# Kernel tuning notes

Hardware: AMD Instinct MI355X
Metric: run time of the kernel (lower is better)

## Reference

```python
import jax, jax.numpy as jnp
import numpy as np

N = 50000   # nodes
E = 800000  # edges (before self loops)
D = 128     # feature dim (n_feat == all n_units due to fusion-cat constraint)
BN_EPS = 1e-5


def _gcn_norm(edge_index, edge_weight, n):
    # PyG gcn_norm with add_self_loops=True (self-loop weight 1.0)
    loop = jnp.arange(n)
    row = jnp.concatenate([edge_index[0], loop])
    col = jnp.concatenate([edge_index[1], loop])
    w = jnp.concatenate([edge_weight, jnp.ones((n,), edge_weight.dtype)])
    deg = jax.ops.segment_sum(w, col, num_segments=n)  # [N]
    deg_safe = jnp.where(deg > 0, deg, 1.0)
    dis = jnp.where(deg > 0, jax.lax.rsqrt(deg_safe), 0.0)
    norm = dis[row] * w * dis[col]  # [E+N]
    return row, col, norm


def _gcn_conv(x, row, col, norm, W, b):
    # out_i = sum_{j->i} norm_ij * (x_j @ W) + b
    h = x @ W                                   # [N, Dout]
    msg = norm[:, None] * h[row]                # gather + scale, [E+N, Dout]
    out = jax.ops.segment_sum(msg, col, num_segments=x.shape[0])
    return out + b


def setup_inputs() -> dict:
    key = jax.random.key(0)
    ks = jax.random.split(key, 9)
    emb = jax.random.normal(ks[0], (N, D), jnp.float32)
    edge_index = jax.random.randint(ks[1], (2, E), 0, N)
    edge_weight = jax.random.uniform(ks[2], (E,), jnp.float32)
    W0 = jax.random.normal(ks[3], (D, D), jnp.float32) / np.sqrt(D).astype(np.float32)
    b0 = jnp.zeros((D,), jnp.float32)
    W1 = jax.random.normal(ks[4], (D, D), jnp.float32) / np.sqrt(D).astype(np.float32)
    b1 = jnp.zeros((D,), jnp.float32)
    bn_gamma = jax.random.uniform(ks[5], (D,), jnp.float32, 0.5, 1.5)
    bn_beta = jax.random.normal(ks[6], (D,), jnp.float32) * 0.1
    bn_mean = jax.random.normal(ks[7], (D,), jnp.float32) * 0.1
    bn_var = jax.random.uniform(ks[8], (D,), jnp.float32, 0.5, 1.5)
    return dict(emb=emb, edge_index=edge_index, edge_weight=edge_weight,
                W0=W0, b0=b0, W1=W1, b1=b1,
                bn_gamma=bn_gamma, bn_beta=bn_beta, bn_mean=bn_mean, bn_var=bn_var)


def reference(emb, edge_index, edge_weight, W0, b0, W1, b1,
              bn_gamma, bn_beta, bn_mean, bn_var):
    n = emb.shape[0]
    row, col, norm = _gcn_norm(edge_index, edge_weight, n)
    # loop runs once (batchnorm_stack has len 1 -> zip truncates):
    h1 = _gcn_conv(emb, row, col, norm, W0, b0)
    h1 = (h1 - bn_mean) * jax.lax.rsqrt(bn_var + BN_EPS) * bn_gamma + bn_beta
    h1 = jax.nn.elu(h1)  # dropout is identity in eval mode
    # final layer applied outside loop, no BN/ELU:
    h2 = _gcn_conv(h1, row, col, norm, W1, b1)
    # fusion: mean over [emb, h1, h2] along the stacked scale axis
    return (emb + h1 + h2) / 3.0
```

## Files before the change

kernel.cpp:

```cpp
#include <hip/hip_runtime.h>
#include <hip/hip_fp16.h>
#include <math.h>

#define BN_EPS 1e-5f
#define CAP 48
#define W_SCALE 68719476736.0f

typedef __attribute__((ext_vector_type(8))) short bf16x8;
typedef __attribute__((ext_vector_type(4))) float f32x4;

__device__ __forceinline__ unsigned short f2b(float f) {
    unsigned u = __float_as_uint(f);
    return (unsigned short)((u + 0x7fffu + ((u >> 16) & 1u)) >> 16);
}
__device__ __forceinline__ unsigned pack2(float lo, float hi) {
    return (unsigned)f2b(lo) | ((unsigned)f2b(hi) << 16);
}
__device__ __forceinline__ float slot_w(unsigned s) {
    return __half2float(__ushort_as_half((unsigned short)(s & 0xffffu)));
}
__device__ __forceinline__ float4 b2f4(ushort4 u) {
    return make_float4(__uint_as_float((unsigned)u.x << 16),
                       __uint_as_float((unsigned)u.y << 16),
                       __uint_as_float((unsigned)u.z << 16),
                       __uint_as_float((unsigned)u.w << 16));
}

__global__ __launch_bounds__(256) void k_prep(
        const int* __restrict__ erow, const int* __restrict__ ecol,
        const float* __restrict__ ew,
        unsigned long long* __restrict__ packed,
        unsigned* __restrict__ eEdge, int E, int SB,
        const float* __restrict__ W0, const float* __restrict__ W1,
        const float* __restrict__ emb,
        unsigned short* __restrict__ wp0, unsigned short* __restrict__ wp1,
        unsigned short* __restrict__ embB, int n) {
    int bb = blockIdx.x;
    if (bb < SB) {
        int e0 = (bb * 256 + threadIdx.x) * 4;
        if (e0 >= E) return;
        if (e0 + 3 < E) {
            int4 r4 = *(const int4*)(erow + e0);
            int4 c4 = *(const int4*)(ecol + e0);
            float4 w4 = *(const float4*)(ew + e0);
            unsigned long long i0 = (1ull << 44) | (unsigned long long)(w4.x * W_SCALE);
            unsigned long long i1 = (1ull << 44) | (unsigned long long)(w4.y * W_SCALE);
            unsigned long long i2 = (1ull << 44) | (unsigned long long)(w4.z * W_SCALE);
            unsigned long long i3 = (1ull << 44) | (unsigned long long)(w4.w * W_SCALE);
            unsigned h0 = __half_as_ushort(__float2half(w4.x));
            unsigned h1 = __half_as_ushort(__float2half(w4.y));
            unsigned h2 = __half_as_ushort(__float2half(w4.z));
            unsigned h3 = __half_as_ushort(__float2half(w4.w));
            unsigned p0 = (unsigned)(atomicAdd(&packed[(size_t)c4.x * 8], i0) >> 44);
            unsigned p1 = (unsigned)(atomicAdd(&packed[(size_t)c4.y * 8], i1) >> 44);
            unsigned p2 = (unsigned)(atomicAdd(&packed[(size_t)c4.z * 8], i2) >> 44);
            unsigned p3 = (unsigned)(atomicAdd(&packed[(size_t)c4.w * 8], i3) >> 44);
            if (p0 < CAP) eEdge[(size_t)c4.x * CAP + p0] = ((unsigned)r4.x << 16) | h0;
            if (p1 < CAP) eEdge[(size_t)c4.y * CAP + p1] = ((unsigned)r4.y << 16) | h1;
            if (p2 < CAP) eEdge[(size_t)c4.z * CAP + p2] = ((unsigned)r4.z << 16) | h2;
            if (p3 < CAP) eEdge[(size_t)c4.w * CAP + p3] = ((unsigned)r4.w << 16) | h3;
        } else {
            for (int e = e0; e < E; ++e) {
                int r = erow[e], c = ecol[e];
                float wv = ew[e];
                unsigned long long inc = (1ull << 44) | (unsigned long long)(wv * W_SCALE);
                unsigned hb = __half_as_ushort(__float2half(wv));
                unsigned p = (unsigned)(atomicAdd(&packed[(size_t)c * 8], inc) >> 44);
                if (p < CAP) eEdge[(size_t)c * CAP + p] = ((unsigned)r << 16) | hb;
            }
        }
    } else {
        int b = bb - SB;
        if (b < 16) {
            int tid = b * 256 + threadIdx.x;
            const float* W = (tid < 2048) ? W0 : W1;
            unsigned short* wp = (tid < 2048) ? wp0 : wp1;
            int f = tid & 2047;
            int q = f >> 9;
            int t = (f >> 6) & 7;
            int l = f & 63;
            int col = t * 16 + (l & 15);
            int k0 = q * 32 + (l >> 4) * 8;
            unsigned short o[8];
            #pragma unroll
            for (int j = 0; j < 8; ++j) o[j] = f2b(W[(k0 + j) * 128 + col]);
            *(uint4*)(wp + (size_t)f * 8) = *(uint4*)o;
        } else {
            int idx = (b - 16) * 256 + threadIdx.x;
            if (idx < n * 16) {
                const float4* src = (const float4*)emb + (size_t)idx * 2;
                float4 v0 = src[0], v1 = src[1];
                uint4 o;
                o.x = pack2(v0.x, v0.y); o.y = pack2(v0.z, v0.w);
                o.z = pack2(v1.x, v1.y); o.w = pack2(v1.z, v1.w);
                ((uint4*)embB)[idx] = o;
            }
        }
    }
}

__global__ __launch_bounds__(256) void k_dis(const unsigned long long* __restrict__ packed,
                                             float* __restrict__ dis,
                                             int* __restrict__ cnt, int n) {
    int i = blockIdx.x * 256 + threadIdx.x;
    if (i >= n) return;
    unsigned long long pk = packed[(size_t)i * 8];
    int c = (int)(pk >> 44);
    if (c > CAP) c = CAP;
    float deg = (float)((double)(pk & ((1ull << 44) - 1)) * (1.0 / 68719476736.0));
    dis[i] = rsqrtf(deg + 1.0f);
    cnt[i] = c;
}

__device__ __forceinline__ void agg_node(const unsigned* __restrict__ ep,
                                         const unsigned short* __restrict__ h,
                                         const float* __restrict__ dis,
                                         float disc, int c, int lane,
                                         float acc[8]) {
    int g = lane >> 4;
    int fo = (lane & 15) * 8;
    for (int j = 0; j < c; j += 16) {
        unsigned s[4];
        int r[4];
        float d[4], nm[4];
        uint4 u[4];
        #pragma unroll
        for (int k = 0; k < 4; ++k) s[k] = ep[j + 4 * k + g];
        #pragma unroll
        for (int k = 0; k < 4; ++k) r[k] = (j + 4 * k + g < c) ? (int)(s[k] >> 16) : 0;
        #pragma unroll
        for (int k = 0; k < 4; ++k) d[k] = dis[r[k]];
        #pragma unroll
        for (int k = 0; k < 4; ++k) u[k] = *(const uint4*)(h + ((size_t)r[k] << 7) + fo);
        #pragma unroll
        for (int k = 0; k < 4; ++k)
            nm[k] = (j + 4 * k + g < c) ? d[k] * slot_w(s[k]) * disc : 0.f;
        #pragma unroll
        for (int k = 0; k < 4; ++k) {
            acc[0] += nm[k] * __uint_as_float(u[k].x << 16);
            acc[1] += nm[k] * __uint_as_float(u[k].x & 0xffff0000u);
            acc[2] += nm[k] * __uint_as_float(u[k].y << 16);
            acc[3] += nm[k] * __uint_as_float(u[k].y & 0xffff0000u);
            acc[4] += nm[k] * __uint_as_float(u[k].z << 16);
            acc[5] += nm[k] * __uint_as_float(u[k].z & 0xffff0000u);
            acc[6] += nm[k] * __uint_as_float(u[k].w << 16);
            acc[7] += nm[k] * __uint_as_float(u[k].w & 0xffff0000u);
        }
    }
    #pragma unroll
    for (int f = 0; f < 8; ++f) {
        acc[f] += __shfl_xor(acc[f], 16);
        acc[f] += __shfl_xor(acc[f], 32);
    }
}

__global__ __launch_bounds__(1024) void k_conv1(
        const int* __restrict__ cnt, const unsigned* __restrict__ eEdge,
        const unsigned short* __restrict__ embB, const float* __restrict__ dis,
        const unsigned short* __restrict__ wp,
        const float* __restrict__ b0, const float* __restrict__ gamma,
        const float* __restrict__ beta, const float* __restrict__ mean,
        const float* __restrict__ var,
        unsigned short* __restrict__ h1b, int n) {
    __shared__ unsigned short sWp[16384];
    __shared__ unsigned short sA[16 * 136];
    int t = threadIdx.x;
    { uint4* d = (uint4*)sWp; const uint4* s = (const uint4*)wp;
      d[t] = s[t]; d[t + 1024] = s[t + 1024]; }
    int w = t >> 6;
    int lane = t & 63;
    int wid = blockIdx.x * 16 + w;
    bool valid = wid < n;
    int c = valid ? __builtin_amdgcn_readfirstlane(cnt[wid]) : 0;
    float disc = valid ? dis[wid] : 0.f;
    float acc[8] = {};
    agg_node(eEdge + (size_t)wid * CAP, embB, dis, disc, c, lane, acc);
    if (lane < 16) {
        int fo = lane * 8;
        float s2 = disc * disc;
        uint4 hu = make_uint4(0, 0, 0, 0);
        if (valid) hu = *(const uint4*)(embB + ((size_t)wid << 7) + fo);
        acc[0] += s2 * __uint_as_float(hu.x << 16);
        acc[1] += s2 * __uint_as_float(hu.x & 0xffff0000u);
        acc[2] += s2 * __uint_as_float(hu.y << 16);
        acc[3] += s2 * __uint_as_float(hu.y & 0xffff0000u);
        acc[4] += s2 * __uint_as_float(hu.z << 16);
        acc[5] += s2 * __uint_as_float(hu.z & 0xffff0000u);
        acc[6] += s2 * __uint_as_float(hu.w << 16);
        acc[7] += s2 * __uint_as_float(hu.w & 0xffff0000u);
        uint4 o;
        o.x = pack2(acc[0], acc[1]); o.y = pack2(acc[2], acc[3]);
        o.z = pack2(acc[4], acc[5]); o.w = pack2(acc[6], acc[7]);
        *(uint4*)(sA + w * 136 + fo) = o;
    }
    __syncthreads();
    int m = lane & 15, quad = lane >> 4;
    f32x4 c2 = {0.f, 0.f, 0.f, 0.f};
    if (w < 8) {
        #pragma unroll
        for (int q = 0; q < 4; ++q) {
            bf16x8 a = *(const bf16x8*)(sA + m * 136 + q * 32 + quad * 8);
            bf16x8 b = *(const bf16x8*)(sWp + (size_t)((q * 8 + w) * 64 + lane) * 8);
            c2 = __builtin_amdgcn_mfma_f32_16x16x32_bf16(a, b, c2, 0, 0, 0);
        }
    }
    __syncthreads();
    if (w < 8) {
        int col = w * 16 + m;
        float bias = b0[col];
        float mn = mean[col], bt = beta[col];
        float iv = rsqrtf(var[col] + BN_EPS) * gamma[col];
        #pragma unroll
        for (int r = 0; r < 4; ++r) {
            float x = c2[r] + bias;
            x = (x - mn) * iv + bt;
            x = x > 0.f ? x : expm1f(x);
            sA[(quad * 4 + r) * 136 + col] = f2b(x);
        }
    }
    __syncthreads();
    if (t < 256) {
        int r = t >> 4, c8 = (t & 15) * 8;
        int node = blockIdx.x * 16 + r;
        if (node < n)
            *(uint4*)(h1b + ((size_t)node << 7) + c8) = *(const uint4*)(sA + r * 136 + c8);
    }
}

__global__ __launch_bounds__(1024) void k_conv2(
        const int* __restrict__ cnt, const unsigned* __restrict__ eEdge,
        const unsigned short* __restrict__ h1b, const float* __restrict__ dis,
        const unsigned short* __restrict__ wp,
        const float* __restrict__ b1, const float* __restrict__ emb,
        float* __restrict__ out, int n) {
    __shared__ unsigned short sWp[16384];
    __shared__ unsigned short sA[16 * 136];
    __shared__ float sC[16 * 132];
    int t = threadIdx.x;
    { uint4* d = (uint4*)sWp; const uint4* s = (const uint4*)wp;
      d[t] = s[t]; d[t + 1024] = s[t + 1024]; }
    int w = t >> 6;
    int lane = t & 63;
    int wid = blockIdx.x * 16 + w;
    bool valid = wid < n;
    int c = valid ? __builtin_amdgcn_readfirstlane(cnt[wid]) : 0;
    float disc = valid ? dis[wid] : 0.f;
    float acc[8] = {};
    agg_node(eEdge + (size_t)wid * CAP, h1b, dis, disc, c, lane, acc);
    if (lane < 16) {
        int fo = lane * 8;
        float s2 = disc * disc;
        uint4 hu = make_uint4(0, 0, 0, 0);
        if (valid) hu = *(const uint4*)(h1b + ((size_t)wid << 7) + fo);
        acc[0] += s2 * __uint_as_float(hu.x << 16);
        acc[1] += s2 * __uint_as_float(hu.x & 0xffff0000u);
        acc[2] += s2 * __uint_as_float(hu.y << 16);
        acc[3] += s2 * __uint_as_float(hu.y & 0xffff0000u);
        acc[4] += s2 * __uint_as_float(hu.z << 16);
        acc[5] += s2 * __uint_as_float(hu.z & 0xffff0000u);
        acc[6] += s2 * __uint_as_float(hu.w << 16);
        acc[7] += s2 * __uint_as_float(hu.w & 0xffff0000u);
        uint4 o;
        o.x = pack2(acc[0], acc[1]); o.y = pack2(acc[2], acc[3]);
        o.z = pack2(acc[4], acc[5]); o.w = pack2(acc[6], acc[7]);
        *(uint4*)(sA + w * 136 + fo) = o;
    }
    __syncthreads();
    int m = lane & 15, quad = lane >> 4;
    f32x4 c2 = {0.f, 0.f, 0.f, 0.f};
    if (w < 8) {
        #pragma unroll
        for (int q = 0; q < 4; ++q) {
            bf16x8 a = *(const bf16x8*)(sA + m * 136 + q * 32 + quad * 8);
            bf16x8 b = *(const bf16x8*)(sWp + (size_t)((q * 8 + w) * 64 + lane) * 8);
            c2 = __builtin_amdgcn_mfma_f32_16x16x32_bf16(a, b, c2, 0, 0, 0);
        }
        int col = w * 16 + m;
        float bias = b1[col];
        #pragma unroll
        for (int r = 0; r < 4; ++r)
            sC[(quad * 4 + r) * 132 + col] = c2[r] + bias;
    }
    __syncthreads();
    if (t < 512) {
        int r = t >> 5, c4 = (t & 31) * 4;
        int node = blockIdx.x * 16 + r;
        if (node < n) {
            float4 cc = *(const float4*)(sC + r * 132 + c4);
            float4 ev = *(const float4*)(emb + ((size_t)node << 7) + c4);
            float4 hv = b2f4(*(const ushort4*)(h1b + ((size_t)node << 7) + c4));
            const float third = 1.0f / 3.0f;
            float4 o;
            o.x = (ev.x + hv.x + cc.x) * third;
            o.y = (ev.y + hv.y + cc.y) * third;
            o.z = (ev.z + hv.z + cc.z) * third;
            o.w = (ev.w + hv.w + cc.w) * third;
            *(float4*)(out + ((size_t)node << 7) + c4) = o;
        }
    }
}

extern "C" void kernel_launch(void* const* d_in, const int* in_sizes, int n_in,
                              void* d_out, int out_size, void* d_ws, size_t ws_size,
                              hipStream_t stream) {
    const float* emb   = (const float*)d_in[0];
    const int*   eidx  = (const int*)d_in[1];
    const float* ew    = (const float*)d_in[2];
    const float* W0    = (const float*)d_in[3];
    const float* b0    = (const float*)d_in[4];
    const float* W1    = (const float*)d_in[5];
    const float* b1    = (const float*)d_in[6];
    const float* gamma = (const float*)d_in[7];
    const float* beta  = (const float*)d_in[8];
    const float* mean  = (const float*)d_in[9];
    const float* var   = (const float*)d_in[10];

    const int n = in_sizes[0] / 128;
    const int E = in_sizes[2];
    const int* rowp = eidx;
    const int* colp = eidx + E;

    char* ws = (char*)d_ws;
    unsigned short* embB = (unsigned short*)ws;
    unsigned short* h1b  = (unsigned short*)(ws + (size_t)n * 256);
    char* p = ws + (size_t)n * 512;
    unsigned long long* packed = (unsigned long long*)p;
    float* dis  = (float*)(p + (size_t)n * 64);
    int*   cnt  = (int*)  (p + (size_t)n * 68);
    unsigned short* wp0 = (unsigned short*)(p + (size_t)n * 72);
    unsigned short* wp1 = (unsigned short*)(p + (size_t)n * 72 + 32768);
    unsigned* eEdge = (unsigned*)(p + (size_t)n * 72 + 65536);
    float* outf = (float*)d_out;

    hipMemsetAsync(packed, 0, (size_t)n * 64, stream);

    const int nb = (n + 255) / 256;
    const int SB = (E + 1023) / 1024;
    const int PB = 16 + (n * 16 + 255) / 256;
    const int cb = (n + 15) / 16;

    k_prep<<<SB + PB, 256, 0, stream>>>(rowp, colp, ew, packed, eEdge, E, SB,
                                        W0, W1, emb, wp0, wp1, embB, n);
    k_dis<<<nb, 256, 0, stream>>>(packed, dis, cnt, n);
    k_conv1<<<cb, 1024, 0, stream>>>(cnt, eEdge, embB, dis, wp0,
                                     b0, gamma, beta, mean, var, h1b, n);
    k_conv2<<<cb, 1024, 0, stream>>>(cnt, eEdge, h1b, dis, wp1,
                                     b1, emb, outf, n);
}
```

Before: 242.4 us.

## Replace global-atomic edge bucketing with two-pass LDS binning by destination block

Edge preprocessing no longer scatters into per-node slots with 64-bit global atomics. It first bins each chunk of edges by destination node block (256 nodes) using a shared-memory histogram and prefix scan. A second kernel then builds per-node edge lists and weighted degrees with LDS atomics, one block per node bin. This drops the memset and the separate degree kernel and aims to cut contended global atomics, at the cost of an extra pass over the binned edge records, which reuse the h1 buffer. The degree is now summed in float rather than fixed-point, so its summation order is nondeterministic.

```diff
diff --git a/kernel.cpp b/kernel.cpp
--- a/kernel.cpp
+++ b/kernel.cpp
@@ -4,7 +4,7 @@
 
 #define BN_EPS 1e-5f
 #define CAP 48
-#define W_SCALE 68719476736.0f
+#define ABLK 8192
 
 typedef __attribute__((ext_vector_type(8))) short bf16x8;
 typedef __attribute__((ext_vector_type(4))) float f32x4;
@@ -26,67 +26,100 @@
                        __uint_as_float((unsigned)u.w << 16));
 }
 
-__global__ __launch_bounds__(256) void k_prep(
+__global__ __launch_bounds__(1024) void k_bin(
         const int* __restrict__ erow, const int* __restrict__ ecol,
         const float* __restrict__ ew,
-        unsigned long long* __restrict__ packed,
-        unsigned* __restrict__ eEdge, int E, int SB,
+        uint2* __restrict__ binned, unsigned short* __restrict__ Hs,
+        int E, int NA, int nbins,
         const float* __restrict__ W0, const float* __restrict__ W1,
         const float* __restrict__ emb,
         unsigned short* __restrict__ wp0, unsigned short* __restrict__ wp1,
         unsigned short* __restrict__ embB, int n) {
     int bb = blockIdx.x;
-    if (bb < SB) {
-        int e0 = (bb * 256 + threadIdx.x) * 4;
-        if (e0 >= E) return;
-        if (e0 + 3 < E) {
-            int4 r4 = *(const int4*)(erow + e0);
-            int4 c4 = *(const int4*)(ecol + e0);
-            float4 w4 = *(const float4*)(ew + e0);
-            unsigned long long i0 = (1ull << 44) | (unsigned long long)(w4.x * W_SCALE);
-            unsigned long long i1 = (1ull << 44) | (unsigned long long)(w4.y * W_SCALE);
-            unsigned long long i2 = (1ull << 44) | (unsigned long long)(w4.z * W_SCALE);
-            unsigned long long i3 = (1ull << 44) | (unsigned long long)(w4.w * W_SCALE);
-            unsigned h0 = __half_as_ushort(__float2half(w4.x));
-            unsigned h1 = __half_as_ushort(__float2half(w4.y));
-            unsigned h2 = __half_as_ushort(__float2half(w4.z));
-            unsigned h3 = __half_as_ushort(__float2half(w4.w));
-            unsigned p0 = (unsigned)(atomicAdd(&packed[(size_t)c4.x * 8], i0) >> 44);
-            unsigned p1 = (unsigned)(atomicAdd(&packed[(size_t)c4.y * 8], i1) >> 44);
-            unsigned p2 = (unsigned)(atomicAdd(&packed[(size_t)c4.z * 8], i2) >> 44);
-            unsigned p3 = (unsigned)(atomicAdd(&packed[(size_t)c4.w * 8], i3) >> 44);
-            if (p0 < CAP) eEdge[(size_t)c4.x * CAP + p0] = ((unsigned)r4.x << 16) | h0;
-            if (p1 < CAP) eEdge[(size_t)c4.y * CAP + p1] = ((unsigned)r4.y << 16) | h1;
-            if (p2 < CAP) eEdge[(size_t)c4.z * CAP + p2] = ((unsigned)r4.z << 16) | h2;
-            if (p3 < CAP) eEdge[(size_t)c4.w * CAP + p3] = ((unsigned)r4.w << 16) | h3;
+    int t = threadIdx.x;
+    if (bb < NA) {
+        __shared__ unsigned sHist[256];
+        __shared__ unsigned sStart[257];
+        __shared__ unsigned sCur[256];
+        if (t < 256) sHist[t] = 0;
+        __syncthreads();
+        int base = bb * ABLK;
+        int m = E - base; if (m > ABLK) m = ABLK;
+        int er[8]; int ec[8]; float ewt[8];
+        int i0 = t * 8;
+        if (i0 + 8 <= m) {
+            int4 ra = *(const int4*)(erow + base + i0);
+            int4 rb = *(const int4*)(erow + base + i0 + 4);
+            int4 ca = *(const int4*)(ecol + base + i0);
+            int4 cb = *(const int4*)(ecol + base + i0 + 4);
+            float4 wa = *(const float4*)(ew + base + i0);
+            float4 wb = *(const float4*)(ew + base + i0 + 4);
+            er[0] = ra.x; er[1] = ra.y; er[2] = ra.z; er[3] = ra.w;
+            er[4] = rb.x; er[5] = rb.y; er[6] = rb.z; er[7] = rb.w;
+            ec[0] = ca.x; ec[1] = ca.y; ec[2] = ca.z; ec[3] = ca.w;
+            ec[4] = cb.x; ec[5] = cb.y; ec[6] = cb.z; ec[7] = cb.w;
+            ewt[0] = wa.x; ewt[1] = wa.y; ewt[2] = wa.z; ewt[3] = wa.w;
+            ewt[4] = wb.x; ewt[5] = wb.y; ewt[6] = wb.z; ewt[7] = wb.w;
         } else {
-            for (int e = e0; e < E; ++e) {
-                int r = erow[e], c = ecol[e];
-                float wv = ew[e];
-                unsigned long long inc = (1ull << 44) | (unsigned long long)(wv * W_SCALE);
-                unsigned hb = __half_as_ushort(__float2half(wv));
-                unsigned p = (unsigned)(atomicAdd(&packed[(size_t)c * 8], inc) >> 44);
-                if (p < CAP) eEdge[(size_t)c * CAP + p] = ((unsigned)r << 16) | hb;
+            #pragma unroll
+            for (int k = 0; k < 8; ++k) {
+                int i = i0 + k;
+                if (i < m) { er[k] = erow[base + i]; ec[k] = ecol[base + i]; ewt[k] = ew[base + i]; }
+                else { er[k] = 0; ec[k] = -1; ewt[k] = 0.f; }
             }
         }
+        #pragma unroll
+        for (int k = 0; k < 8; ++k)
+            if (ec[k] >= 0) atomicAdd(&sHist[ec[k] >> 8], 1u);
+        __syncthreads();
+        if (t < 64) {
+            unsigned carry = 0;
+            #pragma unroll
+            for (int c = 0; c < 4; ++c) {
+                unsigned v = sHist[c * 64 + t];
+                unsigned inc = v;
+                #pragma unroll
+                for (int d = 1; d < 64; d <<= 1) {
+                    unsigned y = __shfl_up(inc, d);
+                    if (t >= d) inc += y;
+                }
+                unsigned ex = carry + inc - v;
+                sStart[c * 64 + t] = ex;
+                sCur[c * 64 + t] = ex;
+                carry += __shfl(inc, 63);
+            }
+            if (t == 0) sStart[256] = carry;
+        }
+        __syncthreads();
+        if (t <= nbins) Hs[(size_t)bb * 256 + t] = (unsigned short)sStart[t];
+        #pragma unroll
+        for (int k = 0; k < 8; ++k) {
+            if (ec[k] >= 0) {
+                int bn = ec[k] >> 8;
+                unsigned pos = atomicAdd(&sCur[bn], 1u);
+                binned[(size_t)base + pos] =
+                    make_uint2(((unsigned)er[k] << 8) | ((unsigned)ec[k] & 255u),
+                               __float_as_uint(ewt[k]));
+            }
+        }
     } else {
-        int b = bb - SB;
-        if (b < 16) {
-            int tid = b * 256 + threadIdx.x;
+        int b2 = bb - NA;
+        if (b2 < 4) {
+            int tid = b2 * 1024 + t;
             const float* W = (tid < 2048) ? W0 : W1;
             unsigned short* wp = (tid < 2048) ? wp0 : wp1;
             int f = tid & 2047;
             int q = f >> 9;
-            int t = (f >> 6) & 7;
+            int tt = (f >> 6) & 7;
             int l = f & 63;
-            int col = t * 16 + (l & 15);
+            int col = tt * 16 + (l & 15);
             int k0 = q * 32 + (l >> 4) * 8;
             unsigned short o[8];
             #pragma unroll
             for (int j = 0; j < 8; ++j) o[j] = f2b(W[(k0 + j) * 128 + col]);
             *(uint4*)(wp + (size_t)f * 8) = *(uint4*)o;
         } else {
-            int idx = (b - 16) * 256 + threadIdx.x;
+            int idx = (b2 - 4) * 1024 + t;
             if (idx < n * 16) {
                 const float4* src = (const float4*)emb + (size_t)idx * 2;
                 float4 v0 = src[0], v1 = src[1];
@@ -99,17 +132,43 @@
     }
 }
 
-__global__ __launch_bounds__(256) void k_dis(const unsigned long long* __restrict__ packed,
-                                             float* __restrict__ dis,
-                                             int* __restrict__ cnt, int n) {
-    int i = blockIdx.x * 256 + threadIdx.x;
-    if (i >= n) return;
-    unsigned long long pk = packed[(size_t)i * 8];
-    int c = (int)(pk >> 44);
-    if (c > CAP) c = CAP;
-    float deg = (float)((double)(pk & ((1ull << 44) - 1)) * (1.0 / 68719476736.0));
-    dis[i] = rsqrtf(deg + 1.0f);
-    cnt[i] = c;
+__global__ __launch_bounds__(1024) void k_build(
+        const uint2* __restrict__ binned, const unsigned short* __restrict__ Hs,
+        int NA, unsigned* __restrict__ eEdge, int* __restrict__ cnt,
+        float* __restrict__ dis, int n) {
+    __shared__ unsigned cntL[256];
+    __shared__ float wsumL[256];
+    int t = threadIdx.x;
+    if (t < 256) { cntL[t] = 0; wsumL[t] = 0.f; }
+    __syncthreads();
+    int b = blockIdx.x;
+    int node0 = b << 8;
+    int wv = t >> 6, lane = t & 63;
+    for (int s = wv; s < NA; s += 16) {
+        int start = Hs[(size_t)s * 256 + b];
+        int end   = Hs[(size_t)s * 256 + b + 1];
+        size_t sb = (size_t)s * ABLK;
+        for (int o = start + lane; o < end; o += 64) {
+            uint2 rec = binned[sb + o];
+            unsigned d = rec.x & 255u;
+            unsigned r = rec.x >> 8;
+            float w = __uint_as_float(rec.y);
+            unsigned p = atomicAdd(&cntL[d], 1u);
+            if (p < CAP)
+                eEdge[(size_t)(node0 + (int)d) * CAP + p] =
+                    (r << 16) | (unsigned)__half_as_ushort(__float2half(w));
+            atomicAdd(&wsumL[d], w);
+        }
+    }
+    __syncthreads();
+    if (t < 256) {
+        int node = node0 + t;
+        if (node < n) {
+            unsigned c = cntL[t]; if (c > CAP) c = CAP;
+            cnt[node] = (int)c;
+            dis[node] = rsqrtf(wsumL[t] + 1.0f);
+        }
+    }
 }
 
 __device__ __forceinline__ void agg_node(const unsigned* __restrict__ ep,
@@ -323,25 +382,24 @@
     char* ws = (char*)d_ws;
     unsigned short* embB = (unsigned short*)ws;
     unsigned short* h1b  = (unsigned short*)(ws + (size_t)n * 256);
+    uint2* binned = (uint2*)h1b;
     char* p = ws + (size_t)n * 512;
-    unsigned long long* packed = (unsigned long long*)p;
-    float* dis  = (float*)(p + (size_t)n * 64);
-    int*   cnt  = (int*)  (p + (size_t)n * 68);
-    unsigned short* wp0 = (unsigned short*)(p + (size_t)n * 72);
-    unsigned short* wp1 = (unsigned short*)(p + (size_t)n * 72 + 32768);
-    unsigned* eEdge = (unsigned*)(p + (size_t)n * 72 + 65536);
+    float* dis  = (float*)p;
+    int*   cnt  = (int*)  (p + (size_t)n * 4);
+    unsigned short* wp0 = (unsigned short*)(p + (size_t)n * 8);
+    unsigned short* wp1 = (unsigned short*)(p + (size_t)n * 8 + 32768);
+    unsigned short* Hs  = (unsigned short*)(p + (size_t)n * 8 + 65536);
+    unsigned* eEdge = (unsigned*)(p + (size_t)n * 8 + 131072);
     float* outf = (float*)d_out;
 
-    hipMemsetAsync(packed, 0, (size_t)n * 64, stream);
-
-    const int nb = (n + 255) / 256;
-    const int SB = (E + 1023) / 1024;
-    const int PB = 16 + (n * 16 + 255) / 256;
-    const int cb = (n + 15) / 16;
-
-    k_prep<<<SB + PB, 256, 0, stream>>>(rowp, colp, ew, packed, eEdge, E, SB,
+    const int NA    = (E + ABLK - 1) / ABLK;
+    const int PB    = 4 + (n * 16 + 1023) / 1024;
+    const int nbins = (n + 255) >> 8;
+    const int cb    = (n + 15) / 16;
+
+    k_bin<<<NA + PB, 1024, 0, stream>>>(rowp, colp, ew, binned, Hs, E, NA, nbins,
                                         W0, W1, emb, wp0, wp1, embB, n);
-    k_dis<<<nb, 256, 0, stream>>>(packed, dis, cnt, n);
+    k_build<<<nbins, 1024, 0, stream>>>(binned, Hs, NA, eEdge, cnt, dis, n);
     k_conv1<<<cb, 1024, 0, stream>>>(cnt, eEdge, embB, dis, wp0,
                                      b0, gamma, beta, mean, var, h1b, n);
     k_conv2<<<cb, 1024, 0, stream>>>(cnt, eEdge, h1b, dis, wp1,
```

Measured after the change: 199.7 us. 1.21x faster.
